# Kernel tuning notes

Hardware: AMD Instinct MI355X
Metric: run time of the kernel (lower is better)

## Reference

```python
import jax, jax.numpy as jnp
import numpy as np

HEADS = 16

def setup_inputs() -> dict:
    key = jax.random.key(0)
    k1, k2, k3 = jax.random.split(key, 3)
    B, N, C = 4, 4096, 1024
    x = jax.random.normal(k1, (B, N, C), dtype=jnp.float32)
    w_qkv = jax.random.normal(k2, (3 * C, C), dtype=jnp.float32) * (C ** -0.5)
    w_proj = jax.random.normal(k3, (C, C), dtype=jnp.float32) * (C ** -0.5)
    b_proj = jnp.zeros((C,), dtype=jnp.float32)
    return {"x": x, "w_qkv": w_qkv, "w_proj": w_proj, "b_proj": b_proj}

def reference(x, w_qkv, w_proj, b_proj):
    B, N, C = x.shape
    H = HEADS
    D = C // H
    qkv = x @ w_qkv.T                      # [B,N,3C]
    q, k, v = jnp.split(qkv, 3, axis=-1)   # each [B,N,C]
    # b n (h d) -> b h d n
    def to_bhdn(t):
        return t.reshape(B, N, H, D).transpose(0, 2, 3, 1)
    q = jax.nn.relu(to_bhdn(q))
    k = jax.nn.relu(to_bhdn(k))
    v = to_bhdn(v)
    eps = jnp.finfo(q.dtype).eps
    ksum = k.sum(axis=-1)                                   # [B,H,D]
    z = 1.0 / (jnp.einsum('bhd,bhdn->bhn', ksum, q) + eps)  # [B,H,N]
    context = jnp.einsum('bhdn,bhen->bhde', v, k)            # v @ k^T, [B,H,D,D]
    out = jnp.einsum('bhde,bhen->bhdn', context, q)          # [B,H,D,N]
    out = out * z[:, :, None, :]
    # b h d n -> b n (h d)
    out = out.transpose(0, 3, 1, 2).reshape(B, N, C)
    return out @ w_proj.T + b_proj
```

## Files before the change

### kernel.cpp

```cpp
#include <hip/hip_runtime.h>
#include <hip/hip_bf16.h>


typedef __bf16 bf16;
typedef __bf16 bf16x8 __attribute__((ext_vector_type(8)));
typedef __bf16 bf16x4 __attribute__((ext_vector_type(4)));
typedef float  f32x4  __attribute__((ext_vector_type(4)));

#define MFMA16(a, b, c) __builtin_amdgcn_mfma_f32_16x16x32_bf16((a), (b), (c), 0, 0, 0)

__device__ __forceinline__ void gload_lds16(const bf16* g, bf16* l) {
  __builtin_amdgcn_global_load_lds(
      (const __attribute__((address_space(1))) void*)g,
      (__attribute__((address_space(3))) void*)l, 16, 0, 0);
}

__global__ __launch_bounds__(256) void cvt3(const float* __restrict__ x,  bf16* __restrict__ xb,
                                            const float* __restrict__ wq, bf16* __restrict__ wqb,
                                            const float* __restrict__ wp, bf16* __restrict__ wpb) {
  const long stride = (long)gridDim.x * 256;
  for (long i4 = (long)blockIdx.x * 256 + threadIdx.x; i4 < 5242880; i4 += stride) {
    const float* s; bf16* d; long off;
    if (i4 < 4194304)      { s = x;  d = xb;  off = i4; }
    else if (i4 < 4980736) { s = wq; d = wqb; off = i4 - 4194304; }
    else                   { s = wp; d = wpb; off = i4 - 4980736; }
    const float4 v = *(const float4*)(s + off * 4);
    bf16x4 o;
    o[0] = (bf16)v.x; o[1] = (bf16)v.y; o[2] = (bf16)v.z; o[3] = (bf16)v.w;
    *(bf16x4*)(d + off * 4) = o;
  }
}

template <int LDC, typename CO>
__global__ __launch_bounds__(256) void gemm_bt3(const bf16* __restrict__ A,
                                                const bf16* __restrict__ Bm,
                                                CO* __restrict__ Co,
                                                const float* __restrict__ bias,
                                                const int reluRows) {
  __shared__ bf16 As[3][128 * 32];
  __shared__ bf16 Bs[3][128 * 32];
  const int tid  = threadIdx.x;
  const int lane = tid & 63;
  const int w    = tid >> 6;
  const int wr   = w >> 1;
  const int wc   = w & 1;
  const int i0 = blockIdx.y * 128;
  const int j0 = blockIdx.x * 128;

  const int srow = lane >> 2;
  const int scol = (lane & 3) * 8;
  const bf16* Ag = A  + (long)(i0 + w * 32 + srow) * 1024 + scol;
  const bf16* Bg = Bm + (long)(j0 + w * 32 + srow) * 1024 + scol;
  const int wofs = w * 1024;

  const int r15  = lane & 15;
  const int koff = (lane >> 4) * 8;

  f32x4 acc[4][4] = {};

#define STG(kt, bsel)                                            \
  do {                                                           \
    const int kk_ = (kt) * 32;                                   \
    gload_lds16(Ag + kk_,             &As[bsel][wofs]);          \
    gload_lds16(Ag + kk_ + 16 * 1024, &As[bsel][wofs + 512]);    \
    gload_lds16(Bg + kk_,             &Bs[bsel][wofs]);          \
    gload_lds16(Bg + kk_ + 16 * 1024, &Bs[bsel][wofs + 512]);    \
  } while (0)

  STG(0, 0);
  STG(1, 1);

  int cur = 0, nxt = 2;
  for (int kt = 0; kt < 32; ++kt) {
    if (kt < 30) {
      STG(kt + 2, nxt);
      asm volatile("s_waitcnt vmcnt(8)" ::: "memory");
    } else if (kt == 30) {
      asm volatile("s_waitcnt vmcnt(4)" ::: "memory");
    } else {
      asm volatile("s_waitcnt vmcnt(0)" ::: "memory");
    }
    __builtin_amdgcn_s_barrier();
    __builtin_amdgcn_sched_barrier(0);

    const bf16* Ab = &As[cur][0];
    const bf16* Bb = &Bs[cur][0];
    bf16x8 af[4], bfm[4];
#pragma unroll
    for (int t = 0; t < 4; ++t)
      af[t] = *(const bf16x8*)(Ab + (wr * 64 + t * 16 + r15) * 32 + koff);
#pragma unroll
    for (int u = 0; u < 4; ++u)
      bfm[u] = *(const bf16x8*)(Bb + (wc * 64 + u * 16 + r15) * 32 + koff);
#pragma unroll
    for (int t = 0; t < 4; ++t)
#pragma unroll
      for (int u = 0; u < 4; ++u)
        acc[t][u] = MFMA16(af[t], bfm[u], acc[t][u]);
    __builtin_amdgcn_s_barrier();
    __builtin_amdgcn_sched_barrier(0);

    cur = (cur == 2) ? 0 : cur + 1;
    nxt = (nxt == 2) ? 0 : nxt + 1;
  }
#undef STG

  const bool doRelu = (i0 < reluRows);
  const int rbase = i0 + wr * 64;
  const int cbase = j0 + wc * 64;
#pragma unroll
  for (int t = 0; t < 4; ++t) {
    const int r0 = rbase + t * 16 + (lane >> 4) * 4;
#pragma unroll
    for (int u = 0; u < 4; ++u) {
      const int cc = cbase + u * 16 + r15;
      const float bv = bias ? bias[cc] : 0.0f;
#pragma unroll
      for (int jj = 0; jj < 4; ++jj) {
        float v = acc[t][u][jj] + bv;
        if (doRelu) v = fmaxf(v, 0.0f);
        Co[(long)(r0 + jj) * LDC + cc] = (CO)v;
      }
    }
  }
}

__global__ __launch_bounds__(256) void ctx_kernel(const bf16* __restrict__ QKV,
                                                  float* __restrict__ ctx_part,
                                                  float* __restrict__ ksum_part) {
  __shared__ bf16 Kl[64 * 128];
  __shared__ bf16 Vl[64 * 128];
  const int bh = blockIdx.x;
  const int s  = blockIdx.y;
  const int b  = bh >> 4, h = bh & 15;
  const int tid = threadIdx.x, lane = tid & 63, w = tid >> 6;
  const long ldq = 16384;
  const bf16* Kp = QKV + (long)(1024 + h * 64) * ldq + b * 4096 + s * 512;
  const bf16* Vp = QKV + (long)(2048 + h * 64) * ldq + b * 4096 + s * 512;
  const int r15 = lane & 15, g = lane >> 4;
  const int x7 = r15 & 7;

  long soff[4]; int dofs[4];
#pragma unroll
  for (int j = 0; j < 4; ++j) {
    const int row = w * 16 + j * 4 + g;
    soff[j] = (long)row * ldq + ((lane & 15) ^ (row & 7)) * 8;
    dofs[j] = (w * 16 + j * 4) * 128;
  }
  const int vrow = (w * 16 + r15) * 128;

  bf16x8 ones;
#pragma unroll
  for (int i = 0; i < 8; ++i) ones[i] = (bf16)1.0f;

  f32x4 acc[4]   = {};
  f32x4 accks[4] = {};

  for (int cc = 0; cc < 4; ++cc) {
#pragma unroll
    for (int j = 0; j < 4; ++j) {
      gload_lds16(Kp + soff[j] + cc * 128, Kl + dofs[j]);
      gload_lds16(Vp + soff[j] + cc * 128, Vl + dofs[j]);
    }
    __syncthreads();
#pragma unroll
    for (int nk = 0; nk < 4; ++nk) {
      const int ch = ((nk * 4 + g) ^ x7) * 8;
      const bf16x8 av = *(const bf16x8*)(Vl + vrow + ch);
#pragma unroll
      for (int u = 0; u < 4; ++u) {
        const bf16x8 kb = *(const bf16x8*)(Kl + (u * 16 + r15) * 128 + ch);
        acc[u]   = MFMA16(av,   kb, acc[u]);
        accks[u] = MFMA16(ones, kb, accks[u]);
      }
    }
    __syncthreads();
  }

  float* cp = ctx_part + (long)(bh * 8 + s) * 4096;
#pragma unroll
  for (int u = 0; u < 4; ++u)
#pragma unroll
    for (int jj = 0; jj < 4; ++jj) {
      const int d = w * 16 + g * 4 + jj;
      const int e = u * 16 + r15;
      cp[d * 64 + e] = acc[u][jj];
    }
  if (w == 0 && g == 0) {
#pragma unroll
    for (int u = 0; u < 4; ++u)
      ksum_part[(bh * 8 + s) * 64 + u * 16 + r15] = accks[u][0];
  }
}

__global__ __launch_bounds__(256) void out_kernel(const bf16* __restrict__ QKV,
                                                  const float* __restrict__ ctx_part,
                                                  const float* __restrict__ ksum_part,
                                                  bf16* __restrict__ O) {
  __shared__ bf16 ctx_lds[64 * 88];
  __shared__ bf16 qlds[256 * 80];
  __shared__ float ksum_lds[64];
  __shared__ float zlds[256];

  const int bh = blockIdx.x;
  const int nc = blockIdx.y;
  const int b = bh >> 4, h = bh & 15;
  const int tid = threadIdx.x, lane = tid & 63, w = tid >> 6;
  const int n0 = nc * 256;
  const long ldq = 16384;

  const float* cp = ctx_part + (long)bh * 8 * 4096;
#pragma unroll
  for (int r = 0; r < 16; ++r) {
    const int idx = tid + r * 256;
    float v = 0.0f;
#pragma unroll
    for (int s2 = 0; s2 < 8; ++s2) v += cp[s2 * 4096 + idx];
    ctx_lds[(idx >> 6) * 88 + (idx & 63)] = (bf16)v;
  }
  if (tid < 64) {
    float v = 0.0f;
#pragma unroll
    for (int s2 = 0; s2 < 8; ++s2) v += ksum_part[(bh * 8 + s2) * 64 + tid];
    ksum_lds[tid] = v;
  }
  {
    const bf16* Qp = QKV + (long)(h * 64) * ldq + b * 4096 + n0;
    const int e = tid >> 2, seg = tid & 3;
    const bf16* qr = Qp + (long)e * ldq + seg * 64;
#pragma unroll
    for (int i = 0; i < 64; i += 8) {
      const bf16x8 v = *(const bf16x8*)(qr + i);
#pragma unroll
      for (int jj = 0; jj < 8; ++jj) qlds[(seg * 64 + i + jj) * 80 + e] = v[jj];
    }
  }
  __syncthreads();

  {
    float a = 0.0f;
    const bf16* qrow = qlds + tid * 80;
#pragma unroll
    for (int d0 = 0; d0 < 64; d0 += 8) {
      const bf16x8 qv = *(const bf16x8*)(qrow + d0);
#pragma unroll
      for (int jj = 0; jj < 8; ++jj) a += (float)qv[jj] * ksum_lds[d0 + jj];
    }
    zlds[tid] = 1.0f / (a + 1.1920929e-07f);
  }
  const int r15 = lane & 15;
  const int koff = (lane >> 4) * 8;
  bf16x8 afr[4][2];
#pragma unroll
  for (int t = 0; t < 4; ++t)
#pragma unroll
    for (int s2 = 0; s2 < 2; ++s2)
      afr[t][s2] = *(const bf16x8*)(ctx_lds + (t * 16 + r15) * 88 + s2 * 32 + koff);
  __syncthreads();

#pragma unroll
  for (int nt = 0; nt < 4; ++nt) {
    const int ntile = w * 4 + nt;
    bf16x8 bfr[2];
#pragma unroll
    for (int s2 = 0; s2 < 2; ++s2)
      bfr[s2] = *(const bf16x8*)(qlds + (ntile * 16 + r15) * 80 + s2 * 32 + koff);
    f32x4 accn[4] = {};
#pragma unroll
    for (int t = 0; t < 4; ++t) {
      accn[t] = MFMA16(afr[t][0], bfr[0], accn[t]);
      accn[t] = MFMA16(afr[t][1], bfr[1], accn[t]);
    }
    const int ncol = n0 + ntile * 16 + r15;
    const float zv = zlds[ntile * 16 + r15];
    bf16* orow = O + (long)(b * 4096 + ncol) * 1024 + h * 64;
#pragma unroll
    for (int t = 0; t < 4; ++t) {
      const int d0 = t * 16 + (lane >> 4) * 4;
      bf16x4 pk;
#pragma unroll
      for (int jj = 0; jj < 4; ++jj) pk[jj] = (bf16)(accn[t][jj] * zv);
      *(bf16x4*)(orow + d0) = pk;
    }
  }
}

template <int LDC, typename CO>
__global__ __launch_bounds__(512, 2) void gemm256(const bf16* __restrict__ A,
                                                  const bf16* __restrict__ Bm,
                                                  CO* __restrict__ Co,
                                                  const float* __restrict__ bias,
                                                  const int reluRows) {
  __shared__ bf16 As[2][256 * 64];
  __shared__ bf16 Bs[2][256 * 64];
  const int tid  = threadIdx.x;
  const int lane = tid & 63;
  const int w    = tid >> 6;
  const int wm   = w >> 2;
  const int wn   = w & 3;

  const int gx = gridDim.x, gy = gridDim.y;
  const int nwg = gx * gy;
  const int id  = blockIdx.x + gx * blockIdx.y;
  const int sid = (id & 7) * (nwg >> 3) + (id >> 3);
  int bx, by;
  if (gx < gy) { bx = sid % gx; by = sid / gx; }
  else         { by = sid % gy; bx = sid / gy; }
  const int i0 = by * 256;
  const int j0 = bx * 256;

  const int lr = lane >> 3;
  const int lc = (lane & 7) ^ lr;
  const bf16* Agl = A  + (long)(i0 + 8 * w + lr) * 1024 + lc * 8;
  const bf16* Bgl = Bm + (long)(j0 + 8 * w + lr) * 1024 + lc * 8;
  const int wofs = w * 512;

  const int r15 = lane & 15, g = lane >> 4;
  const int ck[2] = { ((0 + g) ^ (r15 & 7)) * 8, ((4 + g) ^ (r15 & 7)) * 8 };
  const int arow = (wm * 128 + r15) * 64;
  const int brow = (wn * 64 + r15) * 64;

  f32x4 acc[8][4] = {};

#pragma unroll
  for (int q = 0; q < 4; ++q) {
    gload_lds16(Agl + q * 65536, &As[0][q * 4096 + wofs]);
    gload_lds16(Bgl + q * 65536, &Bs[0][q * 4096 + wofs]);
  }

  for (int kt = 0; kt < 16; ++kt) {
    const int cur = kt & 1;
    if (kt < 15) {
      const long ko = (long)(kt + 1) * 64;
#pragma unroll
      for (int q = 0; q < 4; ++q) {
        gload_lds16(Agl + ko + q * 65536, &As[cur ^ 1][q * 4096 + wofs]);
        gload_lds16(Bgl + ko + q * 65536, &Bs[cur ^ 1][q * 4096 + wofs]);
      }
      asm volatile("s_waitcnt vmcnt(8)" ::: "memory");
    } else {
      asm volatile("s_waitcnt vmcnt(0)" ::: "memory");
    }
    __builtin_amdgcn_s_barrier();
    __builtin_amdgcn_sched_barrier(0);

    const bf16* Ab = &As[cur][arow];
    const bf16* Bb = &Bs[cur][brow];
#pragma unroll
    for (int ks = 0; ks < 2; ++ks) {
      bf16x8 af[8], bfr[4];
#pragma unroll
      for (int fm = 0; fm < 8; ++fm)
        af[fm] = *(const bf16x8*)(Ab + fm * 1024 + ck[ks]);
#pragma unroll
      for (int fn = 0; fn < 4; ++fn)
        bfr[fn] = *(const bf16x8*)(Bb + fn * 1024 + ck[ks]);
      __builtin_amdgcn_s_setprio(1);
#pragma unroll
      for (int fm = 0; fm < 8; ++fm)
#pragma unroll
        for (int fn = 0; fn < 4; ++fn)
          acc[fm][fn] = MFMA16(af[fm], bfr[fn], acc[fm][fn]);
      __builtin_amdgcn_s_setprio(0);
    }
    asm volatile("s_waitcnt lgkmcnt(0)" ::: "memory");
    __builtin_amdgcn_sched_barrier(0);
    __builtin_amdgcn_s_barrier();
  }

  const bool doRelu = (i0 < reluRows);
#pragma unroll
  for (int fm = 0; fm < 8; ++fm) {
    const int r0 = i0 + wm * 128 + fm * 16 + g * 4;
#pragma unroll
    for (int fn = 0; fn < 4; ++fn) {
      const int cc = j0 + wn * 64 + fn * 16 + r15;
      const float bv = bias ? bias[cc] : 0.0f;
#pragma unroll
      for (int jj = 0; jj < 4; ++jj) {
        float v = acc[fm][fn][jj] + bv;
        if (doRelu) v = fmaxf(v, 0.0f);
        Co[(long)(r0 + jj) * LDC + cc] = (CO)v;
      }
    }
  }
}

extern "C" void kernel_launch(void* const* d_in, const int* in_sizes, int n_in,
                              void* d_out, int out_size, void* d_ws, size_t ws_size,
                              hipStream_t stream) {
  const float* x      = (const float*)d_in[0];
  const float* w_qkv  = (const float*)d_in[1];
  const float* w_proj = (const float*)d_in[2];
  const float* b_proj = (const float*)d_in[3];
  float* out = (float*)d_out;

  char* ws = (char*)d_ws;
  bf16*  QKV       = (bf16*)ws;
  float* ctx_part  = (float*)(ws + 100663296);
  float* ksum_part = (float*)(ws + 100663296 + 8388608);
  bf16*  xb        = (bf16*)(ws + 109182976);
  bf16*  O         = xb;
  bf16*  wqkvb     = (bf16*)(ws + 109182976 + 33554432);
  bf16*  wprojb    = (bf16*)(ws + 109182976 + 33554432 + 6291456);

  cvt3<<<2048, 256, 0, stream>>>(x, xb, w_qkv, wqkvb, w_proj, wprojb);
  gemm_bt3<16384, bf16><<<dim3(128, 24), 256, 0, stream>>>(wqkvb, xb, QKV, nullptr, 2048);
  ctx_kernel<<<dim3(64, 8), 256, 0, stream>>>(QKV, ctx_part, ksum_part);
  out_kernel<<<dim3(64, 16), 256, 0, stream>>>(QKV, ctx_part, ksum_part, O);
  gemm256<1024, float><<<dim3(4, 64), 512, 0, stream>>>(O, wprojb, out, b_proj, 0);
}
```

Measured before the change: 226.7 us.

## Replace QKV GEMM with 256x256-tile 8-wave kernel using swizzled LDS and interleaved loads

The QKV projection GEMM moves from a 128x128 tile with 4 waves and a triple-buffered K=32 stage to a 256x256 tile with 8 waves, double-buffered K=64 stages split into halves. Global-to-LDS loads are interleaved between MFMA phases, LDS columns are XOR-swizzled to avoid bank conflicts, and MFMA sections run at raised wave priority. The aim is more data reuse per loaded byte and better overlap of memory with compute. The cost is higher register pressure from 128 accumulator floats per thread, and with only 768 blocks the wave count may fall short of filling the device.

```diff
diff --git a/kernel.cpp b/kernel.cpp
--- a/kernel.cpp
+++ b/kernel.cpp
@@ -32,92 +32,135 @@
 }
 
 template <int LDC, typename CO>
-__global__ __launch_bounds__(256) void gemm_bt3(const bf16* __restrict__ A,
-                                                const bf16* __restrict__ Bm,
-                                                CO* __restrict__ Co,
-                                                const float* __restrict__ bias,
-                                                const int reluRows) {
-  __shared__ bf16 As[3][128 * 32];
-  __shared__ bf16 Bs[3][128 * 32];
-  const int tid  = threadIdx.x;
-  const int lane = tid & 63;
-  const int w    = tid >> 6;
-  const int wr   = w >> 1;
-  const int wc   = w & 1;
-  const int i0 = blockIdx.y * 128;
-  const int j0 = blockIdx.x * 128;
-
-  const int srow = lane >> 2;
-  const int scol = (lane & 3) * 8;
-  const bf16* Ag = A  + (long)(i0 + w * 32 + srow) * 1024 + scol;
-  const bf16* Bg = Bm + (long)(j0 + w * 32 + srow) * 1024 + scol;
-  const int wofs = w * 1024;
-
-  const int r15  = lane & 15;
-  const int koff = (lane >> 4) * 8;
-
-  f32x4 acc[4][4] = {};
-
-#define STG(kt, bsel)                                            \
-  do {                                                           \
-    const int kk_ = (kt) * 32;                                   \
-    gload_lds16(Ag + kk_,             &As[bsel][wofs]);          \
-    gload_lds16(Ag + kk_ + 16 * 1024, &As[bsel][wofs + 512]);    \
-    gload_lds16(Bg + kk_,             &Bs[bsel][wofs]);          \
-    gload_lds16(Bg + kk_ + 16 * 1024, &Bs[bsel][wofs + 512]);    \
-  } while (0)
-
-  STG(0, 0);
-  STG(1, 1);
-
-  int cur = 0, nxt = 2;
-  for (int kt = 0; kt < 32; ++kt) {
-    if (kt < 30) {
-      STG(kt + 2, nxt);
-      asm volatile("s_waitcnt vmcnt(8)" ::: "memory");
-    } else if (kt == 30) {
+__global__ __launch_bounds__(512, 2) void gemm8p(const bf16* __restrict__ A,
+                                                 const bf16* __restrict__ Bm,
+                                                 CO* __restrict__ Co,
+                                                 const float* __restrict__ bias,
+                                                 const int reluRows) {
+  __shared__ bf16 As[2][2][8192];
+  __shared__ bf16 Bs[2][2][8192];
+  const int tid = threadIdx.x, lane = tid & 63, w = tid >> 6;
+  const int wm = w >> 2;
+  const int wn = w & 3;
+  const int i0 = blockIdx.y * 256;
+  const int j0 = blockIdx.x * 256;
+
+  const int lr = lane >> 3, lc = (lane & 7) ^ lr;
+  const bf16* Ags = A  + (long)(i0 + w * 16 + lr) * 1024 + lc * 8;
+  const bf16* Bgs = Bm + (long)(j0 + w * 16 + lr) * 1024 + lc * 8;
+  const int ldst = w * 16 * 64;
+
+  const int r15 = lane & 15, g = lane >> 4;
+  const int ck0 = (g ^ (r15 & 7)) * 8;
+  const int ck1 = ((4 + g) ^ (r15 & 7)) * 8;
+  const int bbase = ((wn & 1) * 64 + r15) * 64;
+
+  f32x4 acc[8][4] = {};
+
+#define STG_A(dd, h, kt, q) \
+  gload_lds16(Ags + (long)(h) * 131072 + (q) * 8192 + (kt) * 64, &As[dd][h][ldst + (q) * 512])
+#define STG_B(dd, h, kt, q) \
+  gload_lds16(Bgs + (long)(h) * 131072 + (q) * 8192 + (kt) * 64, &Bs[dd][h][ldst + (q) * 512])
+
+  STG_A(0, 0, 0, 0); STG_A(0, 0, 0, 1);
+  STG_A(0, 1, 0, 0); STG_A(0, 1, 0, 1);
+  STG_B(0, 0, 0, 0); STG_B(0, 0, 0, 1);
+  STG_B(0, 1, 0, 0); STG_B(0, 1, 0, 1);
+
+  for (int t = 0; t < 16; ++t) {
+    const int d = t & 1, e = d ^ 1;
+    const bf16* Ah = &As[d][wm][0];
+    const bf16* Bh = &Bs[d][wn >> 1][0];
+    bf16x8 af[8], b0, b1;
+
+    if (t < 15) {
+      STG_A(e, 0, t + 1, 0); STG_A(e, 0, t + 1, 1);
+      asm volatile("s_waitcnt vmcnt(4)" ::: "memory");
+    } else {
+      asm volatile("s_waitcnt vmcnt(2)" ::: "memory");
+    }
+    __builtin_amdgcn_s_barrier();
+    __builtin_amdgcn_sched_barrier(0);
+#pragma unroll
+    for (int fm = 0; fm < 8; ++fm)
+      af[fm] = *(const bf16x8*)(Ah + (fm * 16 + r15) * 64 + ck0);
+    b0 = *(const bf16x8*)(Bh + bbase + 0 * 1024 + ck0);
+    b1 = *(const bf16x8*)(Bh + bbase + 1 * 1024 + ck0);
+    asm volatile("s_waitcnt lgkmcnt(0)" ::: "memory");
+    __builtin_amdgcn_sched_barrier(0);
+    __builtin_amdgcn_s_setprio(1);
+#pragma unroll
+    for (int fm = 0; fm < 8; ++fm) {
+      acc[fm][0] = MFMA16(af[fm], b0, acc[fm][0]);
+      acc[fm][1] = MFMA16(af[fm], b1, acc[fm][1]);
+    }
+    __builtin_amdgcn_s_setprio(0);
+
+    if (t < 15) {
+      STG_A(e, 1, t + 1, 0); STG_A(e, 1, t + 1, 1);
       asm volatile("s_waitcnt vmcnt(4)" ::: "memory");
     } else {
       asm volatile("s_waitcnt vmcnt(0)" ::: "memory");
     }
     __builtin_amdgcn_s_barrier();
     __builtin_amdgcn_sched_barrier(0);
-
-    const bf16* Ab = &As[cur][0];
-    const bf16* Bb = &Bs[cur][0];
-    bf16x8 af[4], bfm[4];
-#pragma unroll
-    for (int t = 0; t < 4; ++t)
-      af[t] = *(const bf16x8*)(Ab + (wr * 64 + t * 16 + r15) * 32 + koff);
-#pragma unroll
-    for (int u = 0; u < 4; ++u)
-      bfm[u] = *(const bf16x8*)(Bb + (wc * 64 + u * 16 + r15) * 32 + koff);
-#pragma unroll
-    for (int t = 0; t < 4; ++t)
-#pragma unroll
-      for (int u = 0; u < 4; ++u)
-        acc[t][u] = MFMA16(af[t], bfm[u], acc[t][u]);
+    b0 = *(const bf16x8*)(Bh + bbase + 2 * 1024 + ck0);
+    b1 = *(const bf16x8*)(Bh + bbase + 3 * 1024 + ck0);
+    asm volatile("s_waitcnt lgkmcnt(0)" ::: "memory");
+    __builtin_amdgcn_sched_barrier(0);
+    __builtin_amdgcn_s_setprio(1);
+#pragma unroll
+    for (int fm = 0; fm < 8; ++fm) {
+      acc[fm][2] = MFMA16(af[fm], b0, acc[fm][2]);
+      acc[fm][3] = MFMA16(af[fm], b1, acc[fm][3]);
+    }
+    __builtin_amdgcn_s_setprio(0);
+
+    if (t < 15) { STG_B(e, 0, t + 1, 0); STG_B(e, 0, t + 1, 1); }
+#pragma unroll
+    for (int fm = 0; fm < 8; ++fm)
+      af[fm] = *(const bf16x8*)(Ah + (fm * 16 + r15) * 64 + ck1);
+    b0 = *(const bf16x8*)(Bh + bbase + 0 * 1024 + ck1);
+    b1 = *(const bf16x8*)(Bh + bbase + 1 * 1024 + ck1);
+    asm volatile("s_waitcnt lgkmcnt(0)" ::: "memory");
+    __builtin_amdgcn_sched_barrier(0);
+    __builtin_amdgcn_s_setprio(1);
+#pragma unroll
+    for (int fm = 0; fm < 8; ++fm) {
+      acc[fm][0] = MFMA16(af[fm], b0, acc[fm][0]);
+      acc[fm][1] = MFMA16(af[fm], b1, acc[fm][1]);
+    }
+    __builtin_amdgcn_s_setprio(0);
+
+    if (t < 15) { STG_B(e, 1, t + 1, 0); STG_B(e, 1, t + 1, 1); }
+    b0 = *(const bf16x8*)(Bh + bbase + 2 * 1024 + ck1);
+    b1 = *(const bf16x8*)(Bh + bbase + 3 * 1024 + ck1);
+    asm volatile("s_waitcnt lgkmcnt(0)" ::: "memory");
+    __builtin_amdgcn_sched_barrier(0);
+    __builtin_amdgcn_s_setprio(1);
+#pragma unroll
+    for (int fm = 0; fm < 8; ++fm) {
+      acc[fm][2] = MFMA16(af[fm], b0, acc[fm][2]);
+      acc[fm][3] = MFMA16(af[fm], b1, acc[fm][3]);
+    }
+    __builtin_amdgcn_s_setprio(0);
     __builtin_amdgcn_s_barrier();
     __builtin_amdgcn_sched_barrier(0);
-
-    cur = (cur == 2) ? 0 : cur + 1;
-    nxt = (nxt == 2) ? 0 : nxt + 1;
-  }
-#undef STG
+  }
+#undef STG_A
+#undef STG_B
 
   const bool doRelu = (i0 < reluRows);
-  const int rbase = i0 + wr * 64;
-  const int cbase = j0 + wc * 64;
-#pragma unroll
-  for (int t = 0; t < 4; ++t) {
-    const int r0 = rbase + t * 16 + (lane >> 4) * 4;
-#pragma unroll
-    for (int u = 0; u < 4; ++u) {
-      const int cc = cbase + u * 16 + r15;
+#pragma unroll
+  for (int fm = 0; fm < 8; ++fm) {
+    const int r0 = i0 + wm * 128 + fm * 16 + g * 4;
+#pragma unroll
+    for (int fn = 0; fn < 4; ++fn) {
+      const int cc = j0 + wn * 64 + fn * 16 + r15;
       const float bv = bias ? bias[cc] : 0.0f;
 #pragma unroll
       for (int jj = 0; jj < 4; ++jj) {
-        float v = acc[t][u][jj] + bv;
+        float v = acc[fm][fn][jj] + bv;
         if (doRelu) v = fmaxf(v, 0.0f);
         Co[(long)(r0 + jj) * LDC + cc] = (CO)v;
       }
@@ -405,7 +448,7 @@
   bf16*  wprojb    = (bf16*)(ws + 109182976 + 33554432 + 6291456);
 
   cvt3<<<2048, 256, 0, stream>>>(x, xb, w_qkv, wqkvb, w_proj, wprojb);
-  gemm_bt3<16384, bf16><<<dim3(128, 24), 256, 0, stream>>>(wqkvb, xb, QKV, nullptr, 2048);
+  gemm8p<16384, bf16><<<dim3(64, 12), 512, 0, stream>>>(wqkvb, xb, QKV, nullptr, 2048);
   ctx_kernel<<<dim3(64, 8), 256, 0, stream>>>(QKV, ctx_part, ksum_part);
   out_kernel<<<dim3(64, 16), 256, 0, stream>>>(QKV, ctx_part, ksum_part, O);
   gemm256<1024, float><<<dim3(4, 64), 512, 0, stream>>>(O, wprojb, out, b_proj, 0);
```

Measured after the change: 223.4 us. About the same (-1.5%).
